# Kernel optimization log

Hardware: AMD Instinct MI355X
Metric: run time of the kernel (lower is better)

The kernel has to match this reference:

```python
import jax, jax.numpy as jnp
import numpy as np
from jax import lax

# Model dims (from init_kwargs / mamba_ssm defaults)
D_MODEL = 256
EXPAND = 2
D_INNER = EXPAND * D_MODEL      # 512
D_STATE = 64                     # ssm_rank
DT_RANK = D_MODEL // 16          # 16 (mamba_ssm default ceil(d_model/16))
D_CONV = 4
IMG = 384
PATCH = 16
BATCH = 16
NUM_CLASSES = 10
NBLK = 6                         # sum(depths) = 2+2+2
GRID = IMG // PATCH
NTOK = GRID * GRID + 1           # 577 (patches + cls token)


def setup_inputs() -> dict:
    key = jax.random.key(0)
    ks = iter(jax.random.split(key, 32))
    rn = lambda shape, s=0.02: jax.random.normal(next(ks), shape, jnp.float32) * s
    inp = {}
    inp["x"] = jax.random.normal(next(ks), (BATCH, 3, IMG, IMG), jnp.float32)
    # patch embed conv
    inp["patch_w"] = rn((D_MODEL, 3, PATCH, PATCH), 0.05)
    inp["patch_b"] = jnp.zeros((D_MODEL,), jnp.float32)
    inp["cls_token"] = rn((1, 1, D_MODEL))
    inp["pos_embed"] = rn((1, NTOK, D_MODEL))
    # stacked per-block Mamba params
    inp["norm_w"] = jnp.ones((NBLK, D_MODEL), jnp.float32)
    inp["norm_b"] = jnp.zeros((NBLK, D_MODEL), jnp.float32)
    inp["in_proj_w"] = rn((NBLK, 2 * D_INNER, D_MODEL))
    inp["conv_w"] = rn((NBLK, D_INNER, 1, D_CONV), 0.1)
    inp["conv_b"] = jnp.zeros((NBLK, D_INNER), jnp.float32)
    inp["x_proj_w"] = rn((NBLK, DT_RANK + 2 * D_STATE, D_INNER))
    inp["dt_proj_w"] = rn((NBLK, D_INNER, DT_RANK), 0.1)
    inp["dt_proj_b"] = rn((NBLK, D_INNER), 0.5)
    # S4D-real init: A = -[1..d_state]
    inp["A_log"] = jnp.log(jnp.broadcast_to(
        jnp.arange(1, D_STATE + 1, dtype=jnp.float32), (NBLK, D_INNER, D_STATE)))
    inp["D_ssm"] = jnp.ones((NBLK, D_INNER), jnp.float32)
    inp["out_proj_w"] = rn((NBLK, D_MODEL, D_INNER))
    inp["fnorm_w"] = jnp.ones((D_MODEL,), jnp.float32)
    inp["fnorm_b"] = jnp.zeros((D_MODEL,), jnp.float32)
    inp["head_w"] = rn((NUM_CLASSES, D_MODEL))
    inp["head_b"] = jnp.zeros((NUM_CLASSES,), jnp.float32)
    return inp


def layer_norm(x, w, b, eps=1e-5):
    mu = jnp.mean(x, axis=-1, keepdims=True)
    var = jnp.mean(jnp.square(x - mu), axis=-1, keepdims=True)
    return (x - mu) * lax.rsqrt(var + eps) * w + b


def causal_dwconv(x, w, b):
    # x: (B, di, L), w: (di, 1, K) depthwise; causal left pad K-1
    K = w.shape[-1]
    y = lax.conv_general_dilated(x, w, (1,), [(K - 1, 0)],
                                 dimension_numbers=("NCH", "OIH", "NCH"),
                                 feature_group_count=x.shape[1])
    return y + b[None, :, None]


def selective_scan(u, dt, A, Bm, Cm, Dp):
    # u, dt: (B, L, di); Bm, Cm: (B, L, ds); A: (di, ds); Dp: (di,)
    def step(h, inp):
        dt_t, B_t, C_t, u_t = inp                       # (B,di),(B,ds),(B,ds),(B,di)
        dA = jnp.exp(dt_t[:, :, None] * A)              # (B, di, ds)
        h = dA * h + (dt_t * u_t)[:, :, None] * B_t[:, None, :]
        y = jnp.einsum('bds,bs->bd', h, C_t)
        return h, y
    h0 = jnp.zeros((u.shape[0], A.shape[0], A.shape[1]), u.dtype)
    _, ys = lax.scan(step, h0, (dt.transpose(1, 0, 2), Bm.transpose(1, 0, 2),
                                Cm.transpose(1, 0, 2), u.transpose(1, 0, 2)))
    return ys.transpose(1, 0, 2) + u * Dp


def mamba_block(x, nw, nb, inw, cw, cb, xpw, dtw, dtb, alog, dp, ow):
    res = x
    x = layer_norm(x, nw, nb)
    xz = jnp.einsum('bld,ed->ble', x, inw)              # (B, L, 2*di)
    xi, z = jnp.split(xz, 2, axis=-1)
    xi = causal_dwconv(xi.transpose(0, 2, 1), cw, cb).transpose(0, 2, 1)
    xi = jax.nn.silu(xi)
    dbl = jnp.einsum('bld,ed->ble', xi, xpw)            # (B, L, dt_rank + 2*ds)
    dtr = dbl[..., :DT_RANK]
    Bm = dbl[..., DT_RANK:DT_RANK + D_STATE]
    Cm = dbl[..., DT_RANK + D_STATE:]
    dt = jax.nn.softplus(jnp.einsum('blr,dr->bld', dtr, dtw) + dtb)
    A = -jnp.exp(alog)
    y = selective_scan(xi, dt, A, Bm, Cm, dp)
    y = y * jax.nn.silu(z)
    return res + jnp.einsum('bld,ed->ble', y, ow)


def reference(x, patch_w, patch_b, cls_token, pos_embed,
              norm_w, norm_b, in_proj_w, conv_w, conv_b, x_proj_w,
              dt_proj_w, dt_proj_b, A_log, D_ssm, out_proj_w,
              fnorm_w, fnorm_b, head_w, head_b):
    B = x.shape[0]
    h = lax.conv_general_dilated(x, patch_w, (PATCH, PATCH), 'VALID',
                                 dimension_numbers=("NCHW", "OIHW", "NCHW"))
    h = h + patch_b[None, :, None, None]
    h = h.reshape(B, D_MODEL, -1).transpose(0, 2, 1)    # (B, G*G, D)
    h = jnp.concatenate([jnp.broadcast_to(cls_token, (B, 1, D_MODEL)), h], axis=1)
    h = h + pos_embed
    for i in range(NBLK):
        h = mamba_block(h, norm_w[i], norm_b[i], in_proj_w[i], conv_w[i], conv_b[i],
                        x_proj_w[i], dt_proj_w[i], dt_proj_b[i], A_log[i], D_ssm[i],
                        out_proj_w[i])
    h = layer_norm(h, fnorm_w, fnorm_b)
    return h[:, 0] @ head_w.T + head_b
```

## Files before the change

### kernel.cpp

```cpp
#include <hip/hip_runtime.h>
#include <hip/hip_bf16.h>
#include <cstdint>
#include <cstddef>

#define L_TOK 577
#define DM 256
#define DI 512
#define DS_ 64
#define NROWS (16*577)
#define PROWS (16*576)

typedef float f32x4v __attribute__((ext_vector_type(4)));
typedef __bf16 bf16x8 __attribute__((ext_vector_type(8)));

__device__ __forceinline__ float fast_exp2(float x) {
#if __has_builtin(__builtin_amdgcn_exp2f)
    return __builtin_amdgcn_exp2f(x);
#else
    return __expf(x * 0.6931471805599453f);
#endif
}

__device__ __forceinline__ float dpp_sum64(float x) {
#define DPP_STEP(ctrl) \
    x += __builtin_bit_cast(float, __builtin_amdgcn_update_dpp( \
        0, __builtin_bit_cast(int, x), ctrl, 0xf, 0xf, true))
    DPP_STEP(0x111);
    DPP_STEP(0x112);
    DPP_STEP(0x114);
    DPP_STEP(0x118);
    DPP_STEP(0x142);
    DPP_STEP(0x143);
#undef DPP_STEP
    return x;
}

__global__ __launch_bounds__(256)
void k_gemm(const float* __restrict__ A, int lda,
            const float* __restrict__ B, int ldb,
            float* __restrict__ C, int ldc,
            int M, int N, int K, int beta)
{
    __shared__ char sA[128*64*2];
    __shared__ char sB[128*64*2];
    const int tid  = threadIdx.x;
    const int lane = tid & 63;
    const int wave = tid >> 6;
    const int wr = wave >> 1, wc = wave & 1;
    const int tm = blockIdx.y * 128, tn = blockIdx.x * 128;

    f32x4v acc[4][4];
#pragma unroll
    for (int m = 0; m < 4; ++m)
#pragma unroll
        for (int n = 0; n < 4; ++n) acc[m][n] = (f32x4v){0.f, 0.f, 0.f, 0.f};

    const int nk = K >> 6;
    for (int kt = 0; kt < nk; ++kt) {
        const int k0 = kt << 6;
        __syncthreads();
#pragma unroll
        for (int i = 0; i < 4; ++i) {
            int c = tid + (i << 8);
            int row = c >> 3, slot = c & 7;
            int gr = tm + row; gr = gr < M ? gr : M - 1;
            const float* src = A + (size_t)gr * lda + k0 + (slot << 3);
            float4 lo = *reinterpret_cast<const float4*>(src);
            float4 hi = *reinterpret_cast<const float4*>(src + 4);
            bf16x8 pk;
            pk[0]=(__bf16)lo.x; pk[1]=(__bf16)lo.y; pk[2]=(__bf16)lo.z; pk[3]=(__bf16)lo.w;
            pk[4]=(__bf16)hi.x; pk[5]=(__bf16)hi.y; pk[6]=(__bf16)hi.z; pk[7]=(__bf16)hi.w;
            *reinterpret_cast<bf16x8*>(&sA[(row << 7) + ((slot ^ (row & 7)) << 4)]) = pk;
        }
#pragma unroll
        for (int i = 0; i < 4; ++i) {
            int c = tid + (i << 8);
            int row = c >> 3, slot = c & 7;
            int gr = tn + row; gr = gr < N ? gr : N - 1;
            const float* src = B + (size_t)gr * ldb + k0 + (slot << 3);
            float4 lo = *reinterpret_cast<const float4*>(src);
            float4 hi = *reinterpret_cast<const float4*>(src + 4);
            bf16x8 pk;
            pk[0]=(__bf16)lo.x; pk[1]=(__bf16)lo.y; pk[2]=(__bf16)lo.z; pk[3]=(__bf16)lo.w;
            pk[4]=(__bf16)hi.x; pk[5]=(__bf16)hi.y; pk[6]=(__bf16)hi.z; pk[7]=(__bf16)hi.w;
            *reinterpret_cast<bf16x8*>(&sB[(row << 7) + ((slot ^ (row & 7)) << 4)]) = pk;
        }
        __syncthreads();

        bf16x8 af[4][2], bfr[4][2];
#pragma unroll
        for (int kk = 0; kk < 2; ++kk) {
            int sl = (kk << 2) + (lane >> 4);
#pragma unroll
            for (int m = 0; m < 4; ++m) {
                int row = (wr << 6) + (m << 4) + (lane & 15);
                af[m][kk] = *reinterpret_cast<const bf16x8*>(&sA[(row << 7) + ((sl ^ (row & 7)) << 4)]);
            }
#pragma unroll
            for (int n = 0; n < 4; ++n) {
                int row = (wc << 6) + (n << 4) + (lane & 15);
                bfr[n][kk] = *reinterpret_cast<const bf16x8*>(&sB[(row << 7) + ((sl ^ (row & 7)) << 4)]);
            }
        }
#pragma unroll
        for (int kk = 0; kk < 2; ++kk)
#pragma unroll
            for (int m = 0; m < 4; ++m)
#pragma unroll
                for (int n = 0; n < 4; ++n)
                    acc[m][n] = __builtin_amdgcn_mfma_f32_16x16x32_bf16(af[m][kk], bfr[n][kk], acc[m][n], 0, 0, 0);
    }

#pragma unroll
    for (int m = 0; m < 4; ++m) {
        int grow0 = tm + (wr << 6) + (m << 4) + ((lane >> 4) << 2);
#pragma unroll
        for (int n = 0; n < 4; ++n) {
            int gcol = tn + (wc << 6) + (n << 4) + (lane & 15);
            if (gcol < N) {
#pragma unroll
                for (int j = 0; j < 4; ++j) {
                    int grow = grow0 + j;
                    if (grow < M) {
                        size_t o = (size_t)grow * ldc + gcol;
                        float v = acc[m][n][j];
                        if (beta) v += C[o];
                        C[o] = v;
                    }
                }
            }
        }
    }
}

__global__ __launch_bounds__(256)
void k_im2col(const float* __restrict__ x, float* __restrict__ xcol)
{
    int id = blockIdx.x * 256 + threadIdx.x;
    int kh = id & 15;
    int ci = (id >> 4) % 3;
    int row = id / 48;
    int b = row / 576, p = row % 576;
    int py = p / 24, px = p % 24;
    const float* src = x + ((size_t)(b*3 + ci)*384 + py*16 + kh)*384 + px*16;
    float* dst = xcol + (size_t)row*768 + ci*256 + kh*16;
#pragma unroll
    for (int j = 0; j < 4; ++j)
        *reinterpret_cast<float4*>(dst + j*4) = *reinterpret_cast<const float4*>(src + j*4);
}

__global__ __launch_bounds__(256)
void k_assemble(const float* __restrict__ Ctmp, const float* __restrict__ pb,
                const float* __restrict__ cls, const float* __restrict__ pos,
                float* __restrict__ h_tok)
{
    int i4 = blockIdx.x * 256 + threadIdx.x;
    int c4 = i4 & 63;
    int tok = (i4 >> 6) % 577;
    int b = i4 / (577*64);
    float4 pv = *reinterpret_cast<const float4*>(pos + tok*256 + c4*4);
    float4 r;
    if (tok == 0) {
        float4 cv = *reinterpret_cast<const float4*>(cls + c4*4);
        r.x = cv.x + pv.x; r.y = cv.y + pv.y; r.z = cv.z + pv.z; r.w = cv.w + pv.w;
    } else {
        float4 t = *reinterpret_cast<const float4*>(Ctmp + (size_t)(b*576 + tok - 1)*256 + c4*4);
        float4 bb = *reinterpret_cast<const float4*>(pb + c4*4);
        r.x = t.x + bb.x + pv.x; r.y = t.y + bb.y + pv.y;
        r.z = t.z + bb.z + pv.z; r.w = t.w + bb.w + pv.w;
    }
    *reinterpret_cast<float4*>(h_tok + (size_t)i4*4) = r;
}

__global__ __launch_bounds__(256)
void k_ln(const float* __restrict__ X, const float* __restrict__ w,
          const float* __restrict__ bb, float* __restrict__ O)
{
    int lane = threadIdx.x & 63;
    int row = blockIdx.x * 4 + (threadIdx.x >> 6);
    const float4 v = *reinterpret_cast<const float4*>(X + (size_t)row*256 + lane*4);
    float s1 = v.x + v.y + v.z + v.w;
    float s2 = v.x*v.x + v.y*v.y + v.z*v.z + v.w*v.w;
#pragma unroll
    for (int o2 = 32; o2; o2 >>= 1) { s1 += __shfl_xor(s1, o2); s2 += __shfl_xor(s2, o2); }
    float mu = s1 * (1.f/256.f);
    float var = s2 * (1.f/256.f) - mu*mu;
    float rs = rsqrtf(var + 1e-5f);
    float4 wv = *reinterpret_cast<const float4*>(w + lane*4);
    float4 bv = *reinterpret_cast<const float4*>(bb + lane*4);
    float4 o;
    o.x = (v.x - mu)*rs*wv.x + bv.x;
    o.y = (v.y - mu)*rs*wv.y + bv.y;
    o.z = (v.z - mu)*rs*wv.z + bv.z;
    o.w = (v.w - mu)*rs*wv.w + bv.w;
    *reinterpret_cast<float4*>(O + (size_t)row*256 + lane*4) = o;
}

__global__ __launch_bounds__(256)
void k_conv(const float* __restrict__ xz, const float* __restrict__ cw,
            const float* __restrict__ cb, float* __restrict__ xi)
{
    int gw = blockIdx.x * 4 + (threadIdx.x >> 6);
    int lane = threadIdx.x & 63;
    int tc = gw % 73;
    int eg = (gw / 73) & 7;
    int b  = gw / (73*8);
    int e = eg*64 + lane;
    float4 wv = *reinterpret_cast<const float4*>(cw + e*4);
    float bias = cb[e];
    int t0 = tc * 8;
    float xv[11];
#pragma unroll
    for (int j = 0; j < 11; ++j) {
        int t = t0 - 3 + j;
        xv[j] = (t >= 0 && t < 577) ? xz[(size_t)(b*577 + t)*1024 + e] : 0.f;
    }
#pragma unroll
    for (int j = 0; j < 8; ++j) {
        int t = t0 + j;
        if (t < 577) {
            float a = wv.x*xv[j] + wv.y*xv[j+1] + wv.z*xv[j+2] + wv.w*xv[j+3] + bias;
            float sgm = 1.f / (1.f + __expf(-a));
            xi[(size_t)(b*577 + t)*512 + e] = a * sgm;
        }
    }
}

__global__ __launch_bounds__(256)
void k_dtfuse(const float* __restrict__ dbl, const float* __restrict__ dtw,
              const float* __restrict__ dtb, const float* __restrict__ xi,
              float* __restrict__ tri2)
{
    int row = blockIdx.x >> 1;
    int e = ((blockIdx.x & 1) << 8) + threadIdx.x;
    const float* dr = dbl + (size_t)row*144;
    const float* wp = dtw + e*16;
    float accv = dtb[e];
#pragma unroll
    for (int r = 0; r < 16; r += 4) {
        float4 wv = *reinterpret_cast<const float4*>(wp + r);
        accv += wv.x*dr[r] + wv.y*dr[r+1] + wv.z*dr[r+2] + wv.w*dr[r+3];
    }
    float sp = accv > 20.f ? accv : log1pf(__expf(accv));
    float u = xi[(size_t)row*512 + e];
    float2 o; o.x = sp; o.y = sp * u;
    *reinterpret_cast<float2*>(tri2 + ((size_t)row*512 + e)*2) = o;
}

__global__ __launch_bounds__(256, 8)
void k_scan(const float* __restrict__ tri2, const float* __restrict__ dbl,
            const float* __restrict__ A_log, float* __restrict__ y)
{
    const int lane = threadIdx.x & 63;
    const int wv = __builtin_amdgcn_readfirstlane(threadIdx.x >> 6);
    const int bb = blockIdx.x >> 7;
    const int d  = __builtin_amdgcn_readfirstlane(((blockIdx.x & 127) << 2) + wv);
    const float alog2 = -__expf(A_log[(size_t)d*64 + lane]) * 1.44269504f;
    const size_t row0 = (size_t)bb * 577;
    const float2* trip = reinterpret_cast<const float2*>(tri2) + row0*512 + d;
    const float* Bb = dbl + row0*144 + 16 + lane;
    float* yp = y + row0*512 + d;
    float h = 0.f;
    int t = 0;
    for (; t < 576; t += 4) {
        float p[4];
#pragma unroll
        for (int i = 0; i < 4; ++i) {
            float2 tr = trip[(size_t)(t+i)*512];
            float Bv = Bb[(size_t)(t+i)*144];
            float Cv = Bb[(size_t)(t+i)*144 + 64];
            float dA = fast_exp2(tr.x * alog2);
            h = __builtin_fmaf(dA, h, tr.y * Bv);
            p[i] = h * Cv;
        }
#pragma unroll
        for (int i = 0; i < 4; ++i) p[i] = dpp_sum64(p[i]);
        if (lane == 63) {
#pragma unroll
            for (int i = 0; i < 4; ++i) yp[(size_t)(t+i)*512] = p[i];
        }
    }
    {
        float2 tr = trip[(size_t)t*512];
        float Bv = Bb[(size_t)t*144];
        float Cv = Bb[(size_t)t*144 + 64];
        float dA = fast_exp2(tr.x * alog2);
        h = __builtin_fmaf(dA, h, tr.y * Bv);
        float p = dpp_sum64(h * Cv);
        if (lane == 63) yp[(size_t)t*512] = p;
    }
}

__global__ __launch_bounds__(256)
void k_gate(float* __restrict__ y, const float* __restrict__ xz,
            const float* __restrict__ xi, const float* __restrict__ Dp)
{
    int i4 = blockIdx.x * 256 + threadIdx.x;
    int row = i4 >> 7;
    int c4 = i4 & 127;
    float4 yv = *reinterpret_cast<float4*>(y + (size_t)i4*4);
    float4 uv = *reinterpret_cast<const float4*>(xi + (size_t)i4*4);
    float4 dv = *reinterpret_cast<const float4*>(Dp + c4*4);
    const float4 zv = *reinterpret_cast<const float4*>(xz + (size_t)row*1024 + 512 + c4*4);
    float4 o;
    o.x = (yv.x + uv.x*dv.x) * (zv.x / (1.f + __expf(-zv.x)));
    o.y = (yv.y + uv.y*dv.y) * (zv.y / (1.f + __expf(-zv.y)));
    o.z = (yv.z + uv.z*dv.z) * (zv.z / (1.f + __expf(-zv.z)));
    o.w = (yv.w + uv.w*dv.w) * (zv.w / (1.f + __expf(-zv.w)));
    *reinterpret_cast<float4*>(y + (size_t)i4*4) = o;
}

__global__ __launch_bounds__(256)
void k_head(const float* __restrict__ h_tok, const float* __restrict__ fw,
            const float* __restrict__ fb, const float* __restrict__ hw,
            const float* __restrict__ hb, float* __restrict__ out)
{
    int b = blockIdx.x, tid = threadIdx.x;
    __shared__ float sv[256];
    __shared__ float sr[16];
    float v = h_tok[(size_t)b*577*256 + tid];
    float s1 = v, s2 = v*v;
#pragma unroll
    for (int o2 = 32; o2; o2 >>= 1) { s1 += __shfl_xor(s1, o2); s2 += __shfl_xor(s2, o2); }
    int wave = tid >> 6;
    if ((tid & 63) == 0) { sr[wave] = s1; sr[wave + 8] = s2; }
    __syncthreads();
    float t1 = sr[0] + sr[1] + sr[2] + sr[3];
    float t2 = sr[8] + sr[9] + sr[10] + sr[11];
    float mu = t1 * (1.f/256.f);
    float var = t2 * (1.f/256.f) - mu*mu;
    float rs = rsqrtf(var + 1e-5f);
    sv[tid] = (v - mu)*rs*fw[tid] + fb[tid];
    __syncthreads();
    if (tid < 10) {
        float acc = hb[tid];
        for (int d2 = 0; d2 < 256; ++d2) acc += sv[d2]*hw[tid*256 + d2];
        out[b*10 + tid] = acc;
    }
}

extern "C" void kernel_launch(void* const* d_in, const int* in_sizes, int n_in,
                              void* d_out, int out_size, void* d_ws, size_t ws_size,
                              hipStream_t stream)
{
    const float* x         = (const float*)d_in[0];
    const float* patch_w   = (const float*)d_in[1];
    const float* patch_b   = (const float*)d_in[2];
    const float* cls_tok   = (const float*)d_in[3];
    const float* pos_emb   = (const float*)d_in[4];
    const float* norm_w    = (const float*)d_in[5];
    const float* norm_b    = (const float*)d_in[6];
    const float* in_proj_w = (const float*)d_in[7];
    const float* conv_w    = (const float*)d_in[8];
    const float* conv_b    = (const float*)d_in[9];
    const float* x_proj_w  = (const float*)d_in[10];
    const float* dt_proj_w = (const float*)d_in[11];
    const float* dt_proj_b = (const float*)d_in[12];
    const float* A_log     = (const float*)d_in[13];
    const float* D_ssm     = (const float*)d_in[14];
    const float* out_proj_w= (const float*)d_in[15];
    const float* fnorm_w   = (const float*)d_in[16];
    const float* fnorm_b   = (const float*)d_in[17];
    const float* head_w    = (const float*)d_in[18];
    const float* head_b    = (const float*)d_in[19];
    float* out = (float*)d_out;

    char* ws = (char*)d_ws;
    size_t off = 0;
    auto carve = [&](size_t bytes) -> float* {
        float* p = (float*)(ws + off);
        off += (bytes + 255) & ~(size_t)255;
        return p;
    };
    float* h_tok = carve((size_t)NROWS*DM*4);
    float* xln   = carve((size_t)NROWS*DM*4);
    float* xz    = carve((size_t)NROWS*1024*4);
    float* xi    = carve((size_t)NROWS*DI*4);
    float* dbl   = carve((size_t)NROWS*144*4);
    float* tri2  = carve((size_t)NROWS*DI*2*4);
    float* yb    = carve((size_t)NROWS*DI*4);
    float* xcol  = xz;
    float* Ctmp  = xi;

    k_im2col<<<1728, 256, 0, stream>>>(x, xcol);
    {
        dim3 g(2, 72);
        k_gemm<<<g, 256, 0, stream>>>(xcol, 768, patch_w, 768, Ctmp, 256, PROWS, 256, 768, 0);
    }
    k_assemble<<<2308, 256, 0, stream>>>(Ctmp, patch_b, cls_tok, pos_emb, h_tok);

    for (int i = 0; i < 6; ++i) {
        k_ln<<<2308, 256, 0, stream>>>(h_tok, norm_w + i*DM, norm_b + i*DM, xln);
        {
            dim3 g(8, 73);
            k_gemm<<<g, 256, 0, stream>>>(xln, DM, in_proj_w + (size_t)i*1024*DM, DM,
                                          xz, 1024, NROWS, 1024, DM, 0);
        }
        k_conv<<<2336, 256, 0, stream>>>(xz, conv_w + (size_t)i*DI*4, conv_b + i*DI, xi);
        {
            dim3 g(2, 73);
            k_gemm<<<g, 256, 0, stream>>>(xi, DI, x_proj_w + (size_t)i*144*DI, DI,
                                          dbl, 144, NROWS, 144, DI, 0);
        }
        k_dtfuse<<<NROWS*2, 256, 0, stream>>>(dbl, dt_proj_w + (size_t)i*DI*16, dt_proj_b + i*DI,
                                              xi, tri2);
        k_scan<<<2048, 256, 0, stream>>>(tri2, dbl, A_log + (size_t)i*DI*DS_, yb);
        k_gate<<<4616, 256, 0, stream>>>(yb, xz, xi, D_ssm + i*DI);
        {
            dim3 g(2, 73);
            k_gemm<<<g, 256, 0, stream>>>(yb, DI, out_proj_w + (size_t)i*DM*DI, DI,
                                          h_tok, DM, NROWS, DM, DI, 1);
        }
    }
    k_head<<<16, 256, 0, stream>>>(h_tok, fnorm_w, fnorm_b, head_w, head_b, out);
}
```

Baseline: 1.833 ms.

## Stage B/C in LDS per chunk and reduce scan outputs via LDS transpose

The selective-scan kernel now loads each 16-timestep chunk of B and C into shared memory once per block, so the four waves (four channels) share those loads. The per-timestep DPP wave reductions are replaced by writing the 16 products per lane into a padded LDS tile and summing it transposed, followed by two shuffles. The aim is to cut redundant global loads and the serial cross-lane reduction cost. In exchange it adds two block barriers per chunk, more LDS use, and a lower occupancy hint in launch bounds.

Measured after the change: 1.886 ms. 1.03x slower.

```diff
diff --git a/kernel.cpp b/kernel.cpp
--- a/kernel.cpp
+++ b/kernel.cpp
@@ -19,20 +19,6 @@
 #else
     return __expf(x * 0.6931471805599453f);
 #endif
-}
-
-__device__ __forceinline__ float dpp_sum64(float x) {
-#define DPP_STEP(ctrl) \
-    x += __builtin_bit_cast(float, __builtin_amdgcn_update_dpp( \
-        0, __builtin_bit_cast(int, x), ctrl, 0xf, 0xf, true))
-    DPP_STEP(0x111);
-    DPP_STEP(0x112);
-    DPP_STEP(0x114);
-    DPP_STEP(0x118);
-    DPP_STEP(0x142);
-    DPP_STEP(0x143);
-#undef DPP_STEP
-    return x;
 }
 
 __global__ __launch_bounds__(256)
@@ -247,47 +233,71 @@
     *reinterpret_cast<float2*>(tri2 + ((size_t)row*512 + e)*2) = o;
 }
 
-__global__ __launch_bounds__(256, 8)
+__global__ __launch_bounds__(256, 6)
 void k_scan(const float* __restrict__ tri2, const float* __restrict__ dbl,
             const float* __restrict__ A_log, float* __restrict__ y)
 {
-    const int lane = threadIdx.x & 63;
-    const int wv = __builtin_amdgcn_readfirstlane(threadIdx.x >> 6);
-    const int bb = blockIdx.x >> 7;
-    const int d  = __builtin_amdgcn_readfirstlane(((blockIdx.x & 127) << 2) + wv);
+    __shared__ float bc[16*128];
+    __shared__ float tp[4*16*65];
+    const int tid  = threadIdx.x;
+    const int lane = tid & 63;
+    const int wv   = tid >> 6;
+    const int bb   = blockIdx.x >> 7;
+    const int d    = __builtin_amdgcn_readfirstlane(((blockIdx.x & 127) << 2) + wv);
     const float alog2 = -__expf(A_log[(size_t)d*64 + lane]) * 1.44269504f;
     const size_t row0 = (size_t)bb * 577;
     const float2* trip = reinterpret_cast<const float2*>(tri2) + row0*512 + d;
-    const float* Bb = dbl + row0*144 + 16 + lane;
+    const float* dblb = dbl + row0*144 + 16;
     float* yp = y + row0*512 + d;
+    float* tpw = tp + wv*(16*65);
+    const int j0 = tid >> 5, q = tid & 31;
     float h = 0.f;
-    int t = 0;
-    for (; t < 576; t += 4) {
-        float p[4];
-#pragma unroll
-        for (int i = 0; i < 4; ++i) {
-            float2 tr = trip[(size_t)(t+i)*512];
-            float Bv = Bb[(size_t)(t+i)*144];
-            float Cv = Bb[(size_t)(t+i)*144 + 64];
+
+    for (int c = 0; c < 36; ++c) {
+        const int t0 = c << 4;
+        __syncthreads();
+        {
+            const float* s0 = dblb + (size_t)(t0 + j0)*144 + q*4;
+            const float* s1 = dblb + (size_t)(t0 + j0 + 8)*144 + q*4;
+            float4 v0 = *reinterpret_cast<const float4*>(s0);
+            float4 v1 = *reinterpret_cast<const float4*>(s1);
+            *reinterpret_cast<float4*>(&bc[j0*128 + q*4]) = v0;
+            *reinterpret_cast<float4*>(&bc[(j0+8)*128 + q*4]) = v1;
+        }
+        __syncthreads();
+        float p[16];
+#pragma unroll
+        for (int j = 0; j < 16; ++j) {
+            float2 tr = trip[(size_t)(t0 + j)*512];
+            float Bv = bc[j*128 + lane];
+            float Cv = bc[j*128 + 64 + lane];
             float dA = fast_exp2(tr.x * alog2);
             h = __builtin_fmaf(dA, h, tr.y * Bv);
-            p[i] = h * Cv;
-        }
-#pragma unroll
-        for (int i = 0; i < 4; ++i) p[i] = dpp_sum64(p[i]);
-        if (lane == 63) {
-#pragma unroll
-            for (int i = 0; i < 4; ++i) yp[(size_t)(t+i)*512] = p[i];
-        }
+            p[j] = h * Cv;
+        }
+#pragma unroll
+        for (int j = 0; j < 16; ++j) tpw[j*65 + lane] = p[j];
+        float partial = 0.f;
+        {
+            const int g = lane >> 4, tt = lane & 15;
+            const float* rp = tpw + tt*65 + g*16;
+#pragma unroll
+            for (int k = 0; k < 16; ++k) partial += rp[k];
+        }
+        partial += __shfl_xor(partial, 16);
+        partial += __shfl_xor(partial, 32);
+        if (lane < 16) yp[(size_t)(t0 + lane)*512] = partial;
     }
     {
-        float2 tr = trip[(size_t)t*512];
-        float Bv = Bb[(size_t)t*144];
-        float Cv = Bb[(size_t)t*144 + 64];
+        float2 tr = trip[(size_t)576*512];
+        float Bv = dblb[(size_t)576*144 + lane];
+        float Cv = dblb[(size_t)576*144 + 64 + lane];
         float dA = fast_exp2(tr.x * alog2);
         h = __builtin_fmaf(dA, h, tr.y * Bv);
-        float p = dpp_sum64(h * Cv);
-        if (lane == 63) yp[(size_t)t*512] = p;
+        float p = h * Cv;
+        p += __shfl_xor(p, 32); p += __shfl_xor(p, 16); p += __shfl_xor(p, 8);
+        p += __shfl_xor(p, 4);  p += __shfl_xor(p, 2);  p += __shfl_xor(p, 1);
+        if (lane == 0) yp[(size_t)576*512] = p;
     }
 }
 
```
